# Performance work log

Hardware: AMD Instinct MI355X
Metric: run time of the kernel (lower is better)

The kernel has to match this reference:

```python
import jax, jax.numpy as jnp
from jax import lax
import numpy as np

IN_DIM, HID, B, T = 8, 50, 4096, 512

def setup_inputs() -> dict:
    key = jax.random.key(0)
    ks = jax.random.split(key, 8)
    s_ih = 1.0 / np.sqrt(HID)
    return {
        "x": jax.random.normal(ks[0], (B, T, IN_DIM), dtype=jnp.float32),
        "W_ih": jax.random.uniform(ks[1], (3 * HID, IN_DIM), jnp.float32, -s_ih, s_ih),
        "W_hh": jax.random.uniform(ks[2], (3 * HID, HID), jnp.float32, -s_ih, s_ih),
        "b_ih": jax.random.uniform(ks[3], (3 * HID,), jnp.float32, -s_ih, s_ih),
        "b_hh": jax.random.uniform(ks[4], (3 * HID,), jnp.float32, -s_ih, s_ih),
        "W_out": jax.random.uniform(ks[5], (1, HID), jnp.float32, -s_ih, s_ih),
        "b_out": jax.random.uniform(ks[6], (1,), jnp.float32, -s_ih, s_ih),
    }

def reference(x, W_ih, W_hh, b_ih, b_hh, W_out, b_out):
    # Precompute input projections for all timesteps: [B, T, 3H]
    xW = jnp.einsum('bti,gi->btg', x, W_ih) + b_ih

    def step(h, xw_t):  # h: [B, H], xw_t: [B, 3H]
        gi_r, gi_z, gi_n = jnp.split(xw_t, 3, axis=-1)
        gh = h @ W_hh.T + b_hh
        gh_r, gh_z, gh_n = jnp.split(gh, 3, axis=-1)
        r = jax.nn.sigmoid(gi_r + gh_r)
        z = jax.nn.sigmoid(gi_z + gh_z)
        n = jnp.tanh(gi_n + r * gh_n)
        h_new = (1.0 - z) * n + z * h
        return h_new, None

    h0 = jnp.zeros((x.shape[0], W_hh.shape[1]), dtype=x.dtype)
    hT, _ = lax.scan(step, h0, jnp.moveaxis(xW, 1, 0))  # scan over time
    # Linear head on final hidden state; torch squeezes the layer dim -> [B, 1]
    return hT @ W_out.T + b_out
```

## Files before the change

### kernel.cpp

```cpp
#include <hip/hip_runtime.h>

#define HID 50
#define IND 8
#define TLEN 512
#define NB 16
#define CH 128
#define XSTR 1032
#define BSTR 72
#define NTILE 13

typedef _Float16 f16x8 __attribute__((ext_vector_type(8)));
typedef _Float16 f16x4 __attribute__((ext_vector_type(4)));
typedef float f32x4 __attribute__((ext_vector_type(4)));

__device__ __forceinline__ float fast_sigmoid(float v) {
    float e = __builtin_amdgcn_exp2f(-1.44269504f * v);
    return __builtin_amdgcn_rcpf(1.0f + e);
}
__device__ __forceinline__ float fast_tanh(float v) {
    float e = __builtin_amdgcn_exp2f(2.88539008f * v);
    return 1.0f - 2.0f * __builtin_amdgcn_rcpf(e + 1.0f);
}

__global__ __launch_bounds__(832, 1) void gru_mfma6(
    const float* __restrict__ x,
    const float* __restrict__ W_ih,
    const float* __restrict__ W_hh,
    const float* __restrict__ b_ih,
    const float* __restrict__ b_hh,
    const float* __restrict__ W_out,
    const float* __restrict__ b_out,
    float* __restrict__ out)
{
    const int tid  = threadIdx.x;
    const int wave = tid >> 6;
    const int lane = tid & 63;
    const int m16  = lane & 15;
    const int quad = lane >> 4;
    const int bb   = blockIdx.x;
    const int jh   = 4 * wave + quad;

    __shared__ _Float16 x_lds[NB * XSTR];
    __shared__ _Float16 B_lds[2][16 * BSTR];
    __shared__ float    red[NB * 56];

    auto aval = [&](int k) -> float {
        const int R  = 16 * wave + m16;
        const int rj = R >> 2;
        const int g  = R & 3;
        if (rj >= HID) return 0.f;
        if (g <= 1) {
            if (k < HID) return W_hh[(g * HID + rj) * HID + k];
            if (k >= 56) return W_ih[(g * HID + rj) * IND + (k - 56)];
            return 0.f;
        }
        if (g == 2) return (k < HID) ? W_hh[(2 * HID + rj) * HID + k] : 0.f;
        return (k >= 56) ? W_ih[(2 * HID + rj) * IND + (k - 56)] : 0.f;
    };

    f16x8 a0, a1;
#pragma unroll
    for (int j = 0; j < 8; ++j) {
        a0[j] = (_Float16)aval(quad * 8 + j);
        a1[j] = (_Float16)aval(32 + quad * 8 + j);
    }
    f32x4 bias;
#pragma unroll
    for (int r = 0; r < 4; ++r) {
        float v = 0.f;
        if (jh < HID) {
            if (r == 0)      v = b_ih[jh] + b_hh[jh];
            else if (r == 1) v = b_ih[HID + jh] + b_hh[HID + jh];
            else if (r == 2) v = b_hh[2 * HID + jh];
            else             v = b_ih[2 * HID + jh];
        }
        bias[r] = v;
    }
    const f32x4 zero4 = {0.f, 0.f, 0.f, 0.f};
    float h = 0.f;

    auto stage_chunk = [&](int c) {
        if (tid < 512) {
            const int n = tid >> 5;
            const int s = tid & 31;
            const float4* src = (const float4*)(x + ((size_t)(bb * NB + n) * TLEN + (size_t)c * CH) * IND);
#pragma unroll
            for (int r = 0; r < 8; ++r) {
                const int fidx = s + 32 * r;
                const float4 v = src[fidx];
                const int trel = fidx >> 1;
                const int d    = (fidx & 1) * 4;
                *(f16x4*)&x_lds[n * XSTR + trel * 8 + d] =
                    f16x4{(_Float16)v.x, (_Float16)v.y, (_Float16)v.z, (_Float16)v.w};
            }
        }
    };

    for (int idx = tid; idx < 2 * 16 * BSTR; idx += 832)
        B_lds[0][idx] = (_Float16)0.f;
    stage_chunk(0);
    __syncthreads();

    auto step = [&](int t, int cur, int nxt) {
        const f16x8 bf0 = *(const f16x8*)&B_lds[cur][m16 * BSTR + quad * 8];
        const _Float16* bf1p = (quad == 3)
            ? &x_lds[m16 * XSTR + (t & (CH - 1)) * 8]
            : &B_lds[cur][m16 * BSTR + 32 + quad * 8];
        const f16x8 bf1 = *(const f16x8*)bf1p;

        const f32x4 c = __builtin_amdgcn_mfma_f32_16x16x32_f16(a0, bf0, bias,  0, 0, 0);
        const f32x4 d = __builtin_amdgcn_mfma_f32_16x16x32_f16(a1, bf1, zero4, 0, 0, 0);

        const float r  = fast_sigmoid(c[0] + d[0]);
        const float z  = fast_sigmoid(c[1] + d[1]);
        const float nn = fast_tanh((c[3] + d[3]) + r * (c[2] + d[2]));
        h = nn + z * (h - nn);
        if (jh < HID)
            B_lds[nxt][m16 * BSTR + jh] = (_Float16)h;
        __syncthreads();
    };

    for (int t2 = 0; t2 < TLEN; t2 += 2) {
        if ((t2 & (CH - 1)) == 0 && t2 != 0) {
            stage_chunk(t2 >> 7);
            __syncthreads();
        }
        step(t2,     0, 1);
        step(t2 + 1, 1, 0);
    }

    if (jh < HID)
        red[m16 * 56 + jh] = h * W_out[jh];
    __syncthreads();
    if (tid < NB) {
        float s = b_out[0];
        for (int j = 0; j < HID; ++j) s += red[tid * 56 + j];
        out[bb * NB + tid] = s;
    }
}

extern "C" void kernel_launch(void* const* d_in, const int* in_sizes, int n_in,
                              void* d_out, int out_size, void* d_ws, size_t ws_size,
                              hipStream_t stream) {
    const float* x     = (const float*)d_in[0];
    const float* W_ih  = (const float*)d_in[1];
    const float* W_hh  = (const float*)d_in[2];
    const float* b_ih  = (const float*)d_in[3];
    const float* b_hh  = (const float*)d_in[4];
    const float* W_out = (const float*)d_in[5];
    const float* b_out = (const float*)d_in[6];
    float* out = (float*)d_out;

    const int B = in_sizes[0] / (TLEN * IND);
    gru_mfma6<<<B / NB, 832, 0, stream>>>(x, W_ih, W_hh, b_ih, b_hh, W_out, b_out, out);
}
```

Measured before the change: 263.8 us.

## Pack two MFMA tiles per wave and shrink the block to 512 threads

```diff
diff --git a/kernel.cpp b/kernel.cpp
--- a/kernel.cpp
+++ b/kernel.cpp
@@ -7,7 +7,7 @@
 #define CH 128
 #define XSTR 1032
 #define BSTR 72
-#define NTILE 13
+#define NTHR 512
 
 typedef _Float16 f16x8 __attribute__((ext_vector_type(8)));
 typedef _Float16 f16x4 __attribute__((ext_vector_type(4)));
@@ -22,7 +22,7 @@
     return 1.0f - 2.0f * __builtin_amdgcn_rcpf(e + 1.0f);
 }
 
-__global__ __launch_bounds__(832, 1) void gru_mfma6(
+__global__ __launch_bounds__(NTHR, 1) void gru_mfma7(
     const float* __restrict__ x,
     const float* __restrict__ W_ih,
     const float* __restrict__ W_hh,
@@ -38,14 +38,18 @@
     const int m16  = lane & 15;
     const int quad = lane >> 4;
     const int bb   = blockIdx.x;
-    const int jh   = 4 * wave + quad;
+
+    const int t0  = 2 * wave;
+    const int t1  = 2 * wave + 1;
+    const int jh0 = 4 * t0 + quad;
+    const int jh1 = 4 * t1 + quad;
 
     __shared__ _Float16 x_lds[NB * XSTR];
     __shared__ _Float16 B_lds[2][16 * BSTR];
     __shared__ float    red[NB * 56];
 
-    auto aval = [&](int k) -> float {
-        const int R  = 16 * wave + m16;
+    auto aval = [&](int tt, int k) -> float {
+        const int R  = 16 * tt + m16;
         const int rj = R >> 2;
         const int g  = R & 3;
         if (rj >= HID) return 0.f;
@@ -58,79 +62,100 @@
         return (k >= 56) ? W_ih[(2 * HID + rj) * IND + (k - 56)] : 0.f;
     };
 
-    f16x8 a0, a1;
+    f16x8 a00, a01, a10, a11;
 #pragma unroll
     for (int j = 0; j < 8; ++j) {
-        a0[j] = (_Float16)aval(quad * 8 + j);
-        a1[j] = (_Float16)aval(32 + quad * 8 + j);
+        a00[j] = (_Float16)aval(t0, quad * 8 + j);
+        a01[j] = (_Float16)aval(t0, 32 + quad * 8 + j);
+        a10[j] = (_Float16)aval(t1, quad * 8 + j);
+        a11[j] = (_Float16)aval(t1, 32 + quad * 8 + j);
     }
-    f32x4 bias;
-#pragma unroll
-    for (int r = 0; r < 4; ++r) {
-        float v = 0.f;
+
+    auto mkbias = [&](int jh) -> f32x4 {
+        f32x4 b = {0.f, 0.f, 0.f, 0.f};
         if (jh < HID) {
-            if (r == 0)      v = b_ih[jh] + b_hh[jh];
-            else if (r == 1) v = b_ih[HID + jh] + b_hh[HID + jh];
-            else if (r == 2) v = b_hh[2 * HID + jh];
-            else             v = b_ih[2 * HID + jh];
+            b[0] = b_ih[jh] + b_hh[jh];
+            b[1] = b_ih[HID + jh] + b_hh[HID + jh];
+            b[2] = b_hh[2 * HID + jh];
+            b[3] = b_ih[2 * HID + jh];
         }
-        bias[r] = v;
-    }
-    const f32x4 zero4 = {0.f, 0.f, 0.f, 0.f};
-    float h = 0.f;
+        return b;
+    };
+    const f32x4 bias0 = mkbias(jh0);
+    const f32x4 bias1 = mkbias(jh1);
+
+    float h0 = 0.f, h1 = 0.f;
 
     auto stage_chunk = [&](int c) {
-        if (tid < 512) {
-            const int n = tid >> 5;
-            const int s = tid & 31;
-            const float4* src = (const float4*)(x + ((size_t)(bb * NB + n) * TLEN + (size_t)c * CH) * IND);
+        const int n = tid >> 5;
+        const int s = tid & 31;
+        const float4* src = (const float4*)(x + ((size_t)(bb * NB + n) * TLEN + (size_t)c * CH) * IND);
 #pragma unroll
-            for (int r = 0; r < 8; ++r) {
-                const int fidx = s + 32 * r;
-                const float4 v = src[fidx];
-                const int trel = fidx >> 1;
-                const int d    = (fidx & 1) * 4;
-                *(f16x4*)&x_lds[n * XSTR + trel * 8 + d] =
-                    f16x4{(_Float16)v.x, (_Float16)v.y, (_Float16)v.z, (_Float16)v.w};
-            }
+        for (int r2 = 0; r2 < 8; ++r2) {
+            const int fidx = s + 32 * r2;
+            const float4 v = src[fidx];
+            const int trel = fidx >> 1;
+            const int d    = (fidx & 1) * 4;
+            *(f16x4*)&x_lds[n * XSTR + trel * 8 + d] =
+                f16x4{(_Float16)v.x, (_Float16)v.y, (_Float16)v.z, (_Float16)v.w};
         }
     };
 
-    for (int idx = tid; idx < 2 * 16 * BSTR; idx += 832)
-        B_lds[0][idx] = (_Float16)0.f;
+    {
+        _Float16* bz = &B_lds[0][0];
+        for (int idx = tid; idx < 2 * 16 * BSTR; idx += NTHR)
+            bz[idx] = (_Float16)0.f;
+    }
     stage_chunk(0);
     __syncthreads();
 
-    auto step = [&](int t, int cur, int nxt) {
-        const f16x8 bf0 = *(const f16x8*)&B_lds[cur][m16 * BSTR + quad * 8];
-        const _Float16* bf1p = (quad == 3)
-            ? &x_lds[m16 * XSTR + (t & (CH - 1)) * 8]
-            : &B_lds[cur][m16 * BSTR + 32 + quad * 8];
-        const f16x8 bf1 = *(const f16x8*)bf1p;
+    const int bq = m16 * BSTR + quad * 8;
+    const int bw = m16 * BSTR;
 
-        const f32x4 c = __builtin_amdgcn_mfma_f32_16x16x32_f16(a0, bf0, bias,  0, 0, 0);
-        const f32x4 d = __builtin_amdgcn_mfma_f32_16x16x32_f16(a1, bf1, zero4, 0, 0, 0);
-
-        const float r  = fast_sigmoid(c[0] + d[0]);
-        const float z  = fast_sigmoid(c[1] + d[1]);
-        const float nn = fast_tanh((c[3] + d[3]) + r * (c[2] + d[2]));
-        h = nn + z * (h - nn);
-        if (jh < HID)
-            B_lds[nxt][m16 * BSTR + jh] = (_Float16)h;
-        __syncthreads();
+    auto gates = [&](const f32x4& cc, float h) -> float {
+        const float r = fast_sigmoid(cc[0]);
+        const float z = fast_sigmoid(cc[1]);
+        const float n = fast_tanh(cc[3] + r * cc[2]);
+        return n + z * (h - n);
     };
 
-    for (int t2 = 0; t2 < TLEN; t2 += 2) {
-        if ((t2 & (CH - 1)) == 0 && t2 != 0) {
-            stage_chunk(t2 >> 7);
-            __syncthreads();
+    for (int c = 0; c < 4; ++c) {
+        if (c != 0) { stage_chunk(c); __syncthreads(); }
+        const _Float16* xb = &x_lds[m16 * XSTR];
+        for (int i = 0; i < CH; i += 2) {
+            {
+                const f16x8 bf0 = *(const f16x8*)&B_lds[0][bq];
+                const f16x8 bf1 = (quad == 3) ? *(const f16x8*)(xb + (size_t)i * 8)
+                                              : *(const f16x8*)&B_lds[0][bq + 32];
+                f32x4 c0 = __builtin_amdgcn_mfma_f32_16x16x32_f16(a00, bf0, bias0, 0, 0, 0);
+                f32x4 c1 = __builtin_amdgcn_mfma_f32_16x16x32_f16(a10, bf0, bias1, 0, 0, 0);
+                c0 = __builtin_amdgcn_mfma_f32_16x16x32_f16(a01, bf1, c0, 0, 0, 0);
+                c1 = __builtin_amdgcn_mfma_f32_16x16x32_f16(a11, bf1, c1, 0, 0, 0);
+                h0 = gates(c0, h0);
+                h1 = gates(c1, h1);
+                B_lds[1][bw + jh0] = (_Float16)h0;
+                B_lds[1][bw + jh1] = (_Float16)h1;
+                __syncthreads();
+            }
+            {
+                const f16x8 bf0 = *(const f16x8*)&B_lds[1][bq];
+                const f16x8 bf1 = (quad == 3) ? *(const f16x8*)(xb + (size_t)(i + 1) * 8)
+                                              : *(const f16x8*)&B_lds[1][bq + 32];
+                f32x4 c0 = __builtin_amdgcn_mfma_f32_16x16x32_f16(a00, bf0, bias0, 0, 0, 0);
+                f32x4 c1 = __builtin_amdgcn_mfma_f32_16x16x32_f16(a10, bf0, bias1, 0, 0, 0);
+                c0 = __builtin_amdgcn_mfma_f32_16x16x32_f16(a01, bf1, c0, 0, 0, 0);
+                c1 = __builtin_amdgcn_mfma_f32_16x16x32_f16(a11, bf1, c1, 0, 0, 0);
+                h0 = gates(c0, h0);
+                h1 = gates(c1, h1);
+                B_lds[0][bw + jh0] = (_Float16)h0;
+                B_lds[0][bw + jh1] = (_Float16)h1;
+                __syncthreads();
+            }
         }
-        step(t2,     0, 1);
-        step(t2 + 1, 1, 0);
     }
 
-    if (jh < HID)
-        red[m16 * 56 + jh] = h * W_out[jh];
+    if (jh0 < HID) red[m16 * 56 + jh0] = h0 * W_out[jh0];
+    if (jh1 < HID) red[m16 * 56 + jh1] = h1 * W_out[jh1];
     __syncthreads();
     if (tid < NB) {
         float s = b_out[0];
@@ -152,5 +177,5 @@
     float* out = (float*)d_out;
 
     const int B = in_sizes[0] / (TLEN * IND);
-    gru_mfma6<<<B / NB, 832, 0, stream>>>(x, W_ih, W_hh, b_ih, b_hh, W_out, b_out, out);
+    gru_mfma7<<<B / NB, NTHR, 0, stream>>>(x, W_ih, W_hh, b_ih, b_hh, W_out, b_out, out);
 }
```

Result: faster. 249.3 us (-5.5%).
